# Performance work log

Measured on AMD Instinct MI355X. Metric: run time of the kernel, lower is better.

## Reference

```python
import jax, jax.numpy as jnp
import numpy as np

DIM_M = 512
NEG_INF = -1e30


def setup_inputs() -> dict:
    key = jax.random.key(0)
    k1, k2, k3, k4, k5, k6, k7 = jax.random.split(key, 7)
    B, Lc, Lq, d = 16, 1024, 512, DIM_M
    C = jax.random.normal(k1, (B, Lc, d), dtype=jnp.float32)
    Q = jax.random.normal(k2, (B, Lq, d), dtype=jnp.float32)
    cmask = jax.random.randint(k3, (B, Lc), 0, 2).astype(jnp.float32)
    qmask = jax.random.randint(k4, (B, Lq), 0, 2).astype(jnp.float32)
    lim = np.sqrt(1.0 / d)
    w = jax.random.uniform(k5, (3 * d,), minval=-lim, maxval=lim, dtype=jnp.float32)
    # out_linear: Linear(4d -> d), torch default init
    bound = np.sqrt(1.0 / (4 * d))
    out_w = jax.random.uniform(k6, (d, 4 * d), minval=-bound, maxval=bound, dtype=jnp.float32)
    out_b = jax.random.uniform(k7, (d,), minval=-bound, maxval=bound, dtype=jnp.float32)
    return {"C": C, "Q": Q, "cmask": cmask, "qmask": qmask, "w": w, "out_w": out_w, "out_b": out_b}


def _mask_logits(t, m):
    return t * m + (1.0 - m) * NEG_INF


def reference(C, Q, cmask, qmask, w, out_w, out_b):
    d = C.shape[-1]
    w1, w2, w3 = w[:d], w[d:2 * d], w[2 * d:]
    # Decomposed trilinear similarity (same math as cat([Ct,Qt,Ct*Qt]) @ w):
    # S[b,i,j] = C[b,i]@w1 + Q[b,j]@w2 + (C[b,i]*w3) @ Q[b,j]
    S = (C @ w1)[:, :, None] + (Q @ w2)[:, None, :] \
        + jnp.einsum('bid,bjd->bij', C * w3, Q)  # [B, Lc, Lq]
    qm = qmask[:, None, :]  # [B, 1, Lq]
    cm = cmask[:, :, None]  # [B, Lc, 1]
    S1 = jax.nn.softmax(_mask_logits(S, qm), axis=2)  # over Lq
    S2 = jax.nn.softmax(_mask_logits(S, cm), axis=1)  # over Lc
    A = jnp.einsum('bij,bjd->bid', S1, Q)  # [B, Lc, d]
    # bmm(bmm(S1, S2^T), C) == S1 @ (S2^T @ C) by associativity (cheaper)
    S2TC = jnp.einsum('bij,bid->bjd', S2, C)  # [B, Lq, d]
    Bm = jnp.einsum('bij,bjd->bid', S1, S2TC)  # [B, Lc, d]
    out = jnp.concatenate([C, A, C * A, C * Bm], axis=2)  # [B, Lc, 4d]
    # dropout inactive (inference); out_linear
    return out @ out_w.T + out_b
```

## Files before the change

kernel.cpp:

```cpp
#include <hip/hip_runtime.h>
#include <hip/hip_bf16.h>


#define NB 16
#define LC 1024
#define LQ 512
#define DM 512
#define D4 2048
#define NEGINF (-1e30f)
#define LDA64 72
#define LDA32 40

typedef __bf16 v8bf __attribute__((ext_vector_type(8)));
typedef __bf16 v4bf __attribute__((ext_vector_type(4)));
typedef float  v4f  __attribute__((ext_vector_type(4)));

#define MFMA16 __builtin_amdgcn_mfma_f32_16x16x32_bf16

#define TILE_SETUP8 \
  const int t = threadIdx.x, lane = t & 63, wave = t >> 6; \
  const int wm = wave >> 2, wn = wave & 3, quad = lane >> 4, col = lane & 15; \
  const int sr = t >> 2;

#define ZERO_ACC8 \
  v4f acc[4][2]; \
  _Pragma("unroll") for (int x = 0; x < 4; ++x) \
  _Pragma("unroll") for (int y = 0; y < 2; ++y) \
  _Pragma("unroll") for (int r = 0; r < 4; ++r) acc[x][y][r] = 0.f;

#define FRAG_MMA8S(AL, BL, LDA, KO) do { \
  v8bf af_[4], bf_[2]; \
  _Pragma("unroll") for (int x = 0; x < 4; ++x) \
    af_[x] = *(const v8bf*)&AL[(wm * 64 + x * 16 + col) * LDA + KO + quad * 8]; \
  _Pragma("unroll") for (int y = 0; y < 2; ++y) \
    bf_[y] = *(const v8bf*)&BL[(wn * 32 + y * 16 + col) * LDA + KO + quad * 8]; \
  _Pragma("unroll") for (int x = 0; x < 4; ++x) \
  _Pragma("unroll") for (int y = 0; y < 2; ++y) \
    acc[x][y] = MFMA16(af_[x], bf_[y], acc[x][y], 0, 0, 0); \
} while (0)

__device__ __forceinline__ void xcd_remap(int& bx, int& by, int& bz) {
  const int gx = gridDim.x, gy = gridDim.y, gz = gridDim.z;
  int flat = bx + gx * (by + gy * bz);
  int per = (gx * gy * gz) >> 3;
  int nw = (flat & 7) * per + (flat >> 3);
  bx = nw % gx;
  int r = nw / gx;
  by = r % gy;
  bz = r / gy;
}

__device__ __forceinline__ v8bf cvt8f(float4 a, float4 b) {
  v8bf h;
  h[0] = (__bf16)a.x; h[1] = (__bf16)a.y; h[2] = (__bf16)a.z; h[3] = (__bf16)a.w;
  h[4] = (__bf16)b.x; h[5] = (__bf16)b.y; h[6] = (__bf16)b.z; h[7] = (__bf16)b.w;
  return h;
}

__global__ void k_rowdots(const float* __restrict__ C, const float* __restrict__ Q,
                          const float* __restrict__ w,
                          float* __restrict__ cw1, float* __restrict__ qw2) {
  const int wid = threadIdx.x >> 6, lane = threadIdx.x & 63;
  const int row = blockIdx.x * 4 + wid;
  const bool isC = row < NB * LC;
  const float* src = isC ? (C + (size_t)row * DM) : (Q + (size_t)(row - NB * LC) * DM);
  const float* wv  = isC ? w : (w + DM);
  float v = 0.f;
#pragma unroll
  for (int tt = 0; tt < 8; ++tt) {
    int k = lane + 64 * tt;
    v += src[k] * wv[k];
  }
#pragma unroll
  for (int off = 32; off; off >>= 1) v += __shfl_down(v, off, 64);
  if (lane == 0) {
    if (isC) cw1[row] = v;
    else     qw2[row - NB * LC] = v;
  }
}

__global__ void k_transpose(const float* __restrict__ in, __bf16* __restrict__ outT,
                            int R, int Cd) {
  __shared__ __bf16 tile[64][66];
  const int b = blockIdx.z;
  const int r0 = blockIdx.y * 64, c0 = blockIdx.x * 64;
  const int tr = threadIdx.x >> 6, tc = threadIdx.x & 63;
  const float* inb = in + (size_t)b * R * Cd;
  __bf16* outb = outT + (size_t)b * Cd * R;
  for (int r = tr; r < 64; r += 4)
    tile[r][tc] = (__bf16)inb[(size_t)(r0 + r) * Cd + c0 + tc];
  __syncthreads();
  for (int c = tr; c < 64; c += 4)
    outb[(size_t)(c0 + c) * R + r0 + tc] = tile[tc][c];
}

__global__ void k_owcvt(const float* __restrict__ OW, __bf16* __restrict__ OWb) {
  size_t i = ((size_t)blockIdx.x * 256 + threadIdx.x) * 4;
  float4 f = *(const float4*)(OW + i);
  v4bf h; h[0] = (__bf16)f.x; h[1] = (__bf16)f.y; h[2] = (__bf16)f.z; h[3] = (__bf16)f.w;
  *(v4bf*)(OWb + i) = h;
}

__global__ __launch_bounds__(512) void k_mfma_S(
    const float* __restrict__ C, const float* __restrict__ Q, const float* __restrict__ w,
    const float* __restrict__ cw1, const float* __restrict__ qw2, float* __restrict__ S) {
  __shared__ __bf16 Al[128 * LDA64], Bl[128 * LDA64];
  int bx = blockIdx.x, by = blockIdx.y, bz = blockIdx.z;
  xcd_remap(bx, by, bz);
  const int b = bz, i0 = by * 128, j0 = bx * 128;
  TILE_SETUP8
  const int skc = (t & 3) * 16;
  const float* Cb = C + (size_t)b * LC * DM;
  const float* Qb = Q + (size_t)b * LQ * DM;
  const float* w3 = w + 2 * DM;
  float4 pc[4], pq[4];
  auto load = [&](int k0) {
    const float* ca = Cb + (size_t)(i0 + sr) * DM + k0 + skc;
    const float* qa = Qb + (size_t)(j0 + sr) * DM + k0 + skc;
#pragma unroll
    for (int u = 0; u < 4; ++u) {
      pc[u] = *(const float4*)(ca + 4 * u);
      pq[u] = *(const float4*)(qa + 4 * u);
    }
  };
  load(0);
  ZERO_ACC8
  for (int k0 = 0; k0 < DM; k0 += 64) {
    const float* wa = w3 + k0 + skc;
#pragma unroll
    for (int u = 0; u < 2; ++u) {
      float4 c0 = pc[2 * u], c1 = pc[2 * u + 1];
      float4 w0 = *(const float4*)(wa + 8 * u), w1 = *(const float4*)(wa + 8 * u + 4);
      v8bf ah;
      ah[0] = (__bf16)(c0.x * w0.x); ah[1] = (__bf16)(c0.y * w0.y);
      ah[2] = (__bf16)(c0.z * w0.z); ah[3] = (__bf16)(c0.w * w0.w);
      ah[4] = (__bf16)(c1.x * w1.x); ah[5] = (__bf16)(c1.y * w1.y);
      ah[6] = (__bf16)(c1.z * w1.z); ah[7] = (__bf16)(c1.w * w1.w);
      *(v8bf*)&Al[sr * LDA64 + skc + 8 * u] = ah;
      *(v8bf*)&Bl[sr * LDA64 + skc + 8 * u] = cvt8f(pq[2 * u], pq[2 * u + 1]);
    }
    __syncthreads();
    int kn = k0 + 64; if (kn >= DM) kn = 0;
    load(kn);
    FRAG_MMA8S(Al, Bl, LDA64, 0);
    FRAG_MMA8S(Al, Bl, LDA64, 32);
    __syncthreads();
  }
  float* Sb = S + (size_t)b * LC * LQ;
#pragma unroll
  for (int x = 0; x < 4; ++x) {
    const int mB = i0 + wm * 64 + x * 16 + quad * 4;
    float cv[4];
#pragma unroll
    for (int r = 0; r < 4; ++r) cv[r] = cw1[b * LC + mB + r];
#pragma unroll
    for (int y = 0; y < 2; ++y) {
      const int j = j0 + wn * 32 + y * 16 + col;
      const float qv = qw2[b * LQ + j];
#pragma unroll
      for (int r = 0; r < 4; ++r)
        Sb[(size_t)(mB + r) * LQ + j] = acc[x][y][r] + cv[r] + qv;
    }
  }
}

__global__ __launch_bounds__(1024) void k_softstat(
    const float* __restrict__ S, const float* __restrict__ qmask,
    const float* __restrict__ cmask, __bf16* __restrict__ S1,
    float2* __restrict__ pstat) {
  __shared__ float2 cst[16][LQ];
  const int b = blockIdx.y, ic = blockIdx.x;
  const int tid = threadIdx.x, wv = tid >> 6, lane = tid & 63;
  const float* qm  = qmask + b * LQ;
  const float* cm  = cmask + b * LC + ic * 64;
  const float* Sb  = S  + ((size_t)b * LC + ic * 64) * LQ;
  __bf16*      S1b = S1 + ((size_t)b * LC + ic * 64) * LQ;
  float colm[8], cols[8];
#pragma unroll
  for (int tt = 0; tt < 8; ++tt) { colm[tt] = -3e38f; cols[tt] = 0.f; }
  for (int it = 0; it < 4; ++it) {
    const int r = wv * 4 + it;
    const float cmv = cm[r];
    const float* Srow = Sb + (size_t)r * LQ;
    float sv[8], l1[8];
    float m = -3e38f;
#pragma unroll
    for (int tt = 0; tt < 8; ++tt) {
      int j = lane + 64 * tt;
      sv[tt] = Srow[j];
      float qv = qm[j];
      l1[tt] = qv * sv[tt] + (1.f - qv) * NEGINF;
      m = fmaxf(m, l1[tt]);
    }
#pragma unroll
    for (int off = 32; off; off >>= 1) m = fmaxf(m, __shfl_xor(m, off, 64));
    float e[8], s = 0.f;
#pragma unroll
    for (int tt = 0; tt < 8; ++tt) { e[tt] = __expf(l1[tt] - m); s += e[tt]; }
#pragma unroll
    for (int off = 32; off; off >>= 1) s += __shfl_xor(s, off, 64);
    const float inv = 1.f / s;
#pragma unroll
    for (int tt = 0; tt < 8; ++tt)
      S1b[(size_t)r * LQ + lane + 64 * tt] = (__bf16)(e[tt] * inv);
#pragma unroll
    for (int tt = 0; tt < 8; ++tt) {
      float l2 = cmv * sv[tt] + (1.f - cmv) * NEGINF;
      if (l2 > colm[tt]) { cols[tt] *= __expf(colm[tt] - l2); colm[tt] = l2; }
      cols[tt] += __expf(l2 - colm[tt]);
    }
  }
#pragma unroll
  for (int tt = 0; tt < 8; ++tt) cst[wv][lane + 64 * tt] = make_float2(colm[tt], cols[tt]);
  __syncthreads();
  if (tid < LQ) {
    float M = -3e38f, Sd = 0.f;
#pragma unroll
    for (int k = 0; k < 16; ++k) {
      float2 p = cst[k][tid];
      float nM = fmaxf(M, p.x);
      Sd = Sd * __expf(M - nM) + p.y * __expf(p.x - nM);
      M = nM;
    }
    pstat[((size_t)(b * 16 + ic) * LQ) + tid] = make_float2(M, Sd);
  }
}

__global__ void k_colwrite(const float* __restrict__ S, const float* __restrict__ cmask,
                           const float2* __restrict__ pstat, __bf16* __restrict__ S2T) {
  __shared__ float Mf[64], If[64];
  __shared__ __bf16 tile[64][66];
  const int b = blockIdx.z, ic = blockIdx.y, j0 = blockIdx.x * 64;
  const int c = threadIdx.x & 63, ip = threadIdx.x >> 6;
  if (threadIdx.x < 64) {
    float M = -3e38f, Sd = 0.f;
#pragma unroll
    for (int k = 0; k < 16; ++k) {
      float2 p = pstat[((size_t)(b * 16 + k) * LQ) + j0 + threadIdx.x];
      float nM = fmaxf(M, p.x);
      Sd = Sd * __expf(M - nM) + p.y * __expf(p.x - nM);
      M = nM;
    }
    Mf[threadIdx.x] = M; If[threadIdx.x] = 1.f / Sd;
  }
  __syncthreads();
  const float M = Mf[c], inv = If[c];
  const float* Sb = S + ((size_t)b * LC + ic * 64) * LQ;
  const float* cm = cmask + b * LC + ic * 64;
  for (int r = ip; r < 64; r += 4) {
    float mk = cm[r];
    float logit = mk * Sb[(size_t)r * LQ + j0 + c] + (1.f - mk) * NEGINF;
    tile[r][c] = (__bf16)(__expf(logit - M) * inv);
  }
  __syncthreads();
  __bf16* S2Tb = S2T + ((size_t)b * LQ + j0) * LC + ic * 64;
  for (int jr = ip; jr < 64; jr += 4)
    S2Tb[(size_t)jr * LC + c] = tile[c][jr];
}

__global__ __launch_bounds__(512) void k_mfma_A(
    const __bf16* __restrict__ S1, const __bf16* __restrict__ QT, __bf16* __restrict__ Aw) {
  __shared__ __bf16 Al[128 * LDA64], Bl[128 * LDA64];
  int bx = blockIdx.x, by = blockIdx.y, bz = blockIdx.z;
  xcd_remap(bx, by, bz);
  const int b = bz, i0 = by * 128, n0 = bx * 128;
  TILE_SETUP8
  const int skc = (t & 3) * 16;
  const __bf16* Ar = S1 + (size_t)b * LC * LQ + (size_t)(i0 + sr) * LQ + skc;
  const __bf16* Br = QT + (size_t)b * DM * LQ + (size_t)(n0 + sr) * LQ + skc;
  v8bf pa0, pa1, pb0, pb1;
  auto load = [&](int k0) {
    pa0 = *(const v8bf*)(Ar + k0); pa1 = *(const v8bf*)(Ar + k0 + 8);
    pb0 = *(const v8bf*)(Br + k0); pb1 = *(const v8bf*)(Br + k0 + 8);
  };
  load(0);
  ZERO_ACC8
  for (int k0 = 0; k0 < LQ; k0 += 64) {
    *(v8bf*)&Al[sr * LDA64 + skc] = pa0; *(v8bf*)&Al[sr * LDA64 + skc + 8] = pa1;
    *(v8bf*)&Bl[sr * LDA64 + skc] = pb0; *(v8bf*)&Bl[sr * LDA64 + skc + 8] = pb1;
    __syncthreads();
    int kn = k0 + 64; if (kn >= LQ) kn = 0;
    load(kn);
    FRAG_MMA8S(Al, Bl, LDA64, 0);
    FRAG_MMA8S(Al, Bl, LDA64, 32);
    __syncthreads();
  }
  __bf16* Ab = Aw + (size_t)b * LC * DM;
#pragma unroll
  for (int x = 0; x < 4; ++x) {
    const int mB = i0 + wm * 64 + x * 16 + quad * 4;
#pragma unroll
    for (int y = 0; y < 2; ++y) {
      const int n = n0 + wn * 32 + y * 16 + col;
#pragma unroll
      for (int r = 0; r < 4; ++r)
        Ab[(size_t)(mB + r) * DM + n] = (__bf16)acc[x][y][r];
    }
  }
}

__global__ __launch_bounds__(512) void k_mfma_T(
    const __bf16* __restrict__ S2T, const __bf16* __restrict__ CT, __bf16* __restrict__ S2TCT) {
  __shared__ __bf16 Al[128 * LDA64], Bl[128 * LDA64];
  int bx = blockIdx.x, by = blockIdx.y, bz = blockIdx.z;
  xcd_remap(bx, by, bz);
  const int b = bz, j0 = by * 128, n0 = bx * 128;
  TILE_SETUP8
  const int skc = (t & 3) * 16;
  const __bf16* Ar = S2T + (size_t)b * LQ * LC + (size_t)(j0 + sr) * LC + skc;
  const __bf16* Br = CT  + (size_t)b * DM * LC + (size_t)(n0 + sr) * LC + skc;
  v8bf pa0, pa1, pb0, pb1;
  auto load = [&](int k0) {
    pa0 = *(const v8bf*)(Ar + k0); pa1 = *(const v8bf*)(Ar + k0 + 8);
    pb0 = *(const v8bf*)(Br + k0); pb1 = *(const v8bf*)(Br + k0 + 8);
  };
  load(0);
  ZERO_ACC8
  for (int k0 = 0; k0 < LC; k0 += 64) {
    *(v8bf*)&Al[sr * LDA64 + skc] = pa0; *(v8bf*)&Al[sr * LDA64 + skc + 8] = pa1;
    *(v8bf*)&Bl[sr * LDA64 + skc] = pb0; *(v8bf*)&Bl[sr * LDA64 + skc + 8] = pb1;
    __syncthreads();
    int kn = k0 + 64; if (kn >= LC) kn = 0;
    load(kn);
    FRAG_MMA8S(Al, Bl, LDA64, 0);
    FRAG_MMA8S(Al, Bl, LDA64, 32);
    __syncthreads();
  }
#pragma unroll
  for (int x = 0; x < 4; ++x) {
    const int jB = j0 + wm * 64 + x * 16 + quad * 4;
#pragma unroll
    for (int y = 0; y < 2; ++y) {
      const int n = n0 + wn * 32 + y * 16 + col;
      v4bf h;
#pragma unroll
      for (int r = 0; r < 4; ++r) h[r] = (__bf16)acc[x][y][r];
      *(v4bf*)&S2TCT[((size_t)b * DM + n) * LQ + jB] = h;
    }
  }
}

__global__ __launch_bounds__(512) void k_mfma_Bm(
    const __bf16* __restrict__ S1, const __bf16* __restrict__ S2TCT, __bf16* __restrict__ Bmw) {
  __shared__ __bf16 Al[128 * LDA64], Bl[128 * LDA64];
  int bx = blockIdx.x, by = blockIdx.y, bz = blockIdx.z;
  xcd_remap(bx, by, bz);
  const int b = bz, i0 = by * 128, n0 = bx * 128;
  TILE_SETUP8
  const int skc = (t & 3) * 16;
  const __bf16* Ar = S1    + (size_t)b * LC * LQ + (size_t)(i0 + sr) * LQ + skc;
  const __bf16* Br = S2TCT + (size_t)b * DM * LQ + (size_t)(n0 + sr) * LQ + skc;
  v8bf pa0, pa1, pb0, pb1;
  auto load = [&](int k0) {
    pa0 = *(const v8bf*)(Ar + k0); pa1 = *(const v8bf*)(Ar + k0 + 8);
    pb0 = *(const v8bf*)(Br + k0); pb1 = *(const v8bf*)(Br + k0 + 8);
  };
  load(0);
  ZERO_ACC8
  for (int k0 = 0; k0 < LQ; k0 += 64) {
    *(v8bf*)&Al[sr * LDA64 + skc] = pa0; *(v8bf*)&Al[sr * LDA64 + skc + 8] = pa1;
    *(v8bf*)&Bl[sr * LDA64 + skc] = pb0; *(v8bf*)&Bl[sr * LDA64 + skc + 8] = pb1;
    __syncthreads();
    int kn = k0 + 64; if (kn >= LQ) kn = 0;
    load(kn);
    FRAG_MMA8S(Al, Bl, LDA64, 0);
    FRAG_MMA8S(Al, Bl, LDA64, 32);
    __syncthreads();
  }
  __bf16* Bb = Bmw + (size_t)b * LC * DM;
#pragma unroll
  for (int x = 0; x < 4; ++x) {
    const int mB = i0 + wm * 64 + x * 16 + quad * 4;
#pragma unroll
    for (int y = 0; y < 2; ++y) {
      const int n = n0 + wn * 32 + y * 16 + col;
#pragma unroll
      for (int r = 0; r < 4; ++r)
        Bb[(size_t)(mB + r) * DM + n] = (__bf16)acc[x][y][r];
    }
  }
}

__global__ __launch_bounds__(512) void k_mfma_out(
    const float* __restrict__ C, const __bf16* __restrict__ Aw, const __bf16* __restrict__ Bmw,
    const __bf16* __restrict__ OWb, const float* __restrict__ ob, float* __restrict__ out) {
  __shared__ __bf16 Asg[4][128 * LDA32], Bsg[4][128 * LDA32];
  int bx = blockIdx.x, by = blockIdx.y, bz = blockIdx.z;
  xcd_remap(bx, by, bz);
  const int b = bz, i0 = by * 128, n0 = bx * 128;
  TILE_SETUP8
  const int skc = (t & 3) * 8;
  const float*  Cr = C   + (size_t)b * LC * DM + (size_t)(i0 + sr) * DM + skc;
  const __bf16* Ar = Aw  + (size_t)b * LC * DM + (size_t)(i0 + sr) * DM + skc;
  const __bf16* Br = Bmw + (size_t)b * LC * DM + (size_t)(i0 + sr) * DM + skc;
  const __bf16* Wr = OWb + (size_t)(n0 + sr) * D4 + skc;
  float4 pc0, pc1; v8bf pA, pB, pw[4];
  auto load = [&](int kl) {
    pc0 = *(const float4*)(Cr + kl); pc1 = *(const float4*)(Cr + kl + 4);
    pA = *(const v8bf*)(Ar + kl);
    pB = *(const v8bf*)(Br + kl);
#pragma unroll
    for (int s = 0; s < 4; ++s) pw[s] = *(const v8bf*)(Wr + s * DM + kl);
  };
  load(0);
  ZERO_ACC8
  for (int kl = 0; kl < DM; kl += 32) {
    float cf[8] = {pc0.x, pc0.y, pc0.z, pc0.w, pc1.x, pc1.y, pc1.z, pc1.w};
    v8bf hC, hCA, hCB;
#pragma unroll
    for (int e = 0; e < 8; ++e) {
      hC[e]  = (__bf16)cf[e];
      hCA[e] = (__bf16)(cf[e] * (float)pA[e]);
      hCB[e] = (__bf16)(cf[e] * (float)pB[e]);
    }
    const int off = sr * LDA32 + skc;
    *(v8bf*)&Asg[0][off] = hC;
    *(v8bf*)&Asg[1][off] = pA;
    *(v8bf*)&Asg[2][off] = hCA;
    *(v8bf*)&Asg[3][off] = hCB;
#pragma unroll
    for (int s = 0; s < 4; ++s) *(v8bf*)&Bsg[s][off] = pw[s];
    __syncthreads();
    int kn = kl + 32; if (kn >= DM) kn = 0;
    load(kn);
#pragma unroll
    for (int s = 0; s < 4; ++s) FRAG_MMA8S(Asg[s], Bsg[s], LDA32, 0);
    __syncthreads();
  }
  float* outb = out + (size_t)b * LC * DM;
#pragma unroll
  for (int x = 0; x < 4; ++x) {
    const int mB = i0 + wm * 64 + x * 16 + quad * 4;
#pragma unroll
    for (int y = 0; y < 2; ++y) {
      const int n = n0 + wn * 32 + y * 16 + col;
      const float bv = ob[n];
#pragma unroll
      for (int r = 0; r < 4; ++r)
        outb[(size_t)(mB + r) * DM + n] = acc[x][y][r] + bv;
    }
  }
}

extern "C" void kernel_launch(void* const* d_in, const int* in_sizes, int n_in,
                              void* d_out, int out_size, void* d_ws, size_t ws_size,
                              hipStream_t stream) {
  const float* C     = (const float*)d_in[0];
  const float* Q     = (const float*)d_in[1];
  const float* cmask = (const float*)d_in[2];
  const float* qmask = (const float*)d_in[3];
  const float* w     = (const float*)d_in[4];
  const float* out_w = (const float*)d_in[5];
  const float* out_b = (const float*)d_in[6];
  float* out = (float*)d_out;

  char* base = (char*)d_ws;
  float*  cw1   = (float*)base;
  float*  qw2   = (float*)(base + 65536);
  char*   R     = base + 131072;
  float*  S     = (float*)R;
  __bf16* Aw    = (__bf16*)R;
  __bf16* CT    = (__bf16*)(R + (16u << 20));
  __bf16* Bmw   = (__bf16*)(R + (16u << 20));
  __bf16* S1    = (__bf16*)(base + 131072 + (32u << 20));
  __bf16* S2T   = (__bf16*)(base + 131072 + (48u << 20));
  __bf16* OWbf  = S2T;
  char*   Z     = base + 131072 + (64u << 20);
  float2* pstat = (float2*)Z;
  __bf16* QT    = (__bf16*)Z;
  __bf16* S2TCT = (__bf16*)Z;
  (void)in_sizes; (void)n_in; (void)out_size; (void)ws_size;

  k_rowdots<<<(NB * LC + NB * LQ) / 4, 256, 0, stream>>>(C, Q, w, cw1, qw2);
  k_mfma_S<<<dim3(LQ / 128, LC / 128, NB), 512, 0, stream>>>(C, Q, w, cw1, qw2, S);
  k_softstat<<<dim3(LC / 64, NB), 1024, 0, stream>>>(S, qmask, cmask, S1, pstat);
  k_colwrite<<<dim3(LQ / 64, LC / 64, NB), 256, 0, stream>>>(S, cmask, pstat, S2T);
  k_transpose<<<dim3(DM / 64, LQ / 64, NB), 256, 0, stream>>>(Q, QT, LQ, DM);
  k_transpose<<<dim3(DM / 64, LC / 64, NB), 256, 0, stream>>>(C, CT, LC, DM);
  k_mfma_A<<<dim3(DM / 128, LC / 128, NB), 512, 0, stream>>>(S1, QT, Aw);
  k_mfma_T<<<dim3(DM / 128, LQ / 128, NB), 512, 0, stream>>>(S2T, CT, S2TCT);
  k_owcvt<<<DM * D4 / 1024, 256, 0, stream>>>(out_w, OWbf);
  k_mfma_Bm<<<dim3(DM / 128, LC / 128, NB), 512, 0, stream>>>(S1, S2TCT, Bmw);
  k_mfma_out<<<dim3(DM / 128, LC / 128, NB), 512, 0, stream>>>(C, Aw, Bmw, OWbf, out_b, out);
}
```

Before: 283.0 us.

## Use direct global-to-LDS loads in shared bf16 GEMM macro with 4x4 wave tiles

```diff
diff --git a/kernel.cpp b/kernel.cpp
--- a/kernel.cpp
+++ b/kernel.cpp
@@ -8,7 +8,6 @@
 #define DM 512
 #define D4 2048
 #define NEGINF (-1e30f)
-#define LDA64 72
 #define LDA32 40
 
 typedef __bf16 v8bf __attribute__((ext_vector_type(8)));
@@ -16,6 +15,10 @@
 typedef float  v4f  __attribute__((ext_vector_type(4)));
 
 #define MFMA16 __builtin_amdgcn_mfma_f32_16x16x32_bf16
+
+#define GLOAD16(gp, lp) __builtin_amdgcn_global_load_lds( \
+    (const __attribute__((address_space(1))) void*)(gp), \
+    (__attribute__((address_space(3))) void*)(lp), 16, 0, 0)
 
 #define TILE_SETUP8 \
   const int t = threadIdx.x, lane = t & 63, wave = t >> 6; \
@@ -39,6 +42,39 @@
     acc[x][y] = MFMA16(af_[x], bf_[y], acc[x][y], 0, 0, 0); \
 } while (0)
 
+#define GEMM_PROLOG \
+  __shared__ __bf16 Al[128 * 64], Bl[128 * 64]; \
+  int bx = blockIdx.x, by = blockIdx.y, bz = blockIdx.z; \
+  xcd_remap(bx, by, bz); \
+  const int b = bz, i0 = by * 128, n0 = bx * 128; \
+  const int t = threadIdx.x, lane = t & 63, wave = t >> 6; \
+  const int wm = wave >> 1, wn = wave & 1, quad = lane >> 4, col = lane & 15; \
+  const int srow = wave * 32 + (lane >> 3), scol = (lane & 7) * 8; \
+  v4f acc[4][4]; \
+  _Pragma("unroll") for (int x = 0; x < 4; ++x) \
+  _Pragma("unroll") for (int y = 0; y < 4; ++y) \
+  _Pragma("unroll") for (int r = 0; r < 4; ++r) acc[x][y][r] = 0.f;
+
+#define GEMM_KLOOP(Arow, Brow, LDGA, LDGB, KEXT) \
+  for (int k0 = 0; k0 < (KEXT); k0 += 64) { \
+    _Pragma("unroll") for (int u = 0; u < 4; ++u) { \
+      GLOAD16(Arow + (size_t)(u * 8) * (LDGA) + k0, &Al[(wave * 32 + u * 8) * 64]); \
+      GLOAD16(Brow + (size_t)(u * 8) * (LDGB) + k0, &Bl[(wave * 32 + u * 8) * 64]); \
+    } \
+    __syncthreads(); \
+    _Pragma("unroll") for (int ko = 0; ko < 2; ++ko) { \
+      v8bf af_[4], bf_[4]; \
+      _Pragma("unroll") for (int x = 0; x < 4; ++x) \
+        af_[x] = *(const v8bf*)&Al[(wm * 64 + x * 16 + col) * 64 + ko * 32 + quad * 8]; \
+      _Pragma("unroll") for (int y = 0; y < 4; ++y) \
+        bf_[y] = *(const v8bf*)&Bl[(wn * 64 + y * 16 + col) * 64 + ko * 32 + quad * 8]; \
+      _Pragma("unroll") for (int x = 0; x < 4; ++x) \
+      _Pragma("unroll") for (int y = 0; y < 4; ++y) \
+        acc[x][y] = MFMA16(af_[x], bf_[y], acc[x][y], 0, 0, 0); \
+    } \
+    __syncthreads(); \
+  }
+
 __device__ __forceinline__ void xcd_remap(int& bx, int& by, int& bz) {
   const int gx = gridDim.x, gy = gridDim.y, gz = gridDim.z;
   int flat = bx + gx * (by + gy * bz);
@@ -59,23 +95,38 @@
 
 __global__ void k_rowdots(const float* __restrict__ C, const float* __restrict__ Q,
                           const float* __restrict__ w,
-                          float* __restrict__ cw1, float* __restrict__ qw2) {
+                          float* __restrict__ cw1, float* __restrict__ qw2,
+                          __bf16* __restrict__ Cbf, __bf16* __restrict__ Qw3) {
   const int wid = threadIdx.x >> 6, lane = threadIdx.x & 63;
   const int row = blockIdx.x * 4 + wid;
   const bool isC = row < NB * LC;
-  const float* src = isC ? (C + (size_t)row * DM) : (Q + (size_t)(row - NB * LC) * DM);
+  const int lr = isC ? row : row - NB * LC;
+  const float* src = (isC ? C : Q) + (size_t)lr * DM;
   const float* wv  = isC ? w : (w + DM);
+  const float* w3  = w + 2 * DM;
+  __bf16* dst = (isC ? Cbf : Qw3) + (size_t)lr * DM;
   float v = 0.f;
 #pragma unroll
-  for (int tt = 0; tt < 8; ++tt) {
-    int k = lane + 64 * tt;
-    v += src[k] * wv[k];
+  for (int s = 0; s < 2; ++s) {
+    const int k = lane * 4 + s * 256;
+    float4 f = *(const float4*)(src + k);
+    float4 g = *(const float4*)(wv + k);
+    v += f.x * g.x + f.y * g.y + f.z * g.z + f.w * g.w;
+    v4bf h;
+    if (isC) {
+      h[0] = (__bf16)f.x; h[1] = (__bf16)f.y; h[2] = (__bf16)f.z; h[3] = (__bf16)f.w;
+    } else {
+      float4 s3 = *(const float4*)(w3 + k);
+      h[0] = (__bf16)(f.x * s3.x); h[1] = (__bf16)(f.y * s3.y);
+      h[2] = (__bf16)(f.z * s3.z); h[3] = (__bf16)(f.w * s3.w);
+    }
+    *(v4bf*)(dst + k) = h;
   }
 #pragma unroll
   for (int off = 32; off; off >>= 1) v += __shfl_down(v, off, 64);
   if (lane == 0) {
     if (isC) cw1[row] = v;
-    else     qw2[row - NB * LC] = v;
+    else     qw2[lr] = v;
   }
 }
 
@@ -101,51 +152,14 @@
   *(v4bf*)(OWb + i) = h;
 }
 
-__global__ __launch_bounds__(512) void k_mfma_S(
-    const float* __restrict__ C, const float* __restrict__ Q, const float* __restrict__ w,
-    const float* __restrict__ cw1, const float* __restrict__ qw2, float* __restrict__ S) {
-  __shared__ __bf16 Al[128 * LDA64], Bl[128 * LDA64];
-  int bx = blockIdx.x, by = blockIdx.y, bz = blockIdx.z;
-  xcd_remap(bx, by, bz);
-  const int b = bz, i0 = by * 128, j0 = bx * 128;
-  TILE_SETUP8
-  const int skc = (t & 3) * 16;
-  const float* Cb = C + (size_t)b * LC * DM;
-  const float* Qb = Q + (size_t)b * LQ * DM;
-  const float* w3 = w + 2 * DM;
-  float4 pc[4], pq[4];
-  auto load = [&](int k0) {
-    const float* ca = Cb + (size_t)(i0 + sr) * DM + k0 + skc;
-    const float* qa = Qb + (size_t)(j0 + sr) * DM + k0 + skc;
-#pragma unroll
-    for (int u = 0; u < 4; ++u) {
-      pc[u] = *(const float4*)(ca + 4 * u);
-      pq[u] = *(const float4*)(qa + 4 * u);
-    }
-  };
-  load(0);
-  ZERO_ACC8
-  for (int k0 = 0; k0 < DM; k0 += 64) {
-    const float* wa = w3 + k0 + skc;
-#pragma unroll
-    for (int u = 0; u < 2; ++u) {
-      float4 c0 = pc[2 * u], c1 = pc[2 * u + 1];
-      float4 w0 = *(const float4*)(wa + 8 * u), w1 = *(const float4*)(wa + 8 * u + 4);
-      v8bf ah;
-      ah[0] = (__bf16)(c0.x * w0.x); ah[1] = (__bf16)(c0.y * w0.y);
-      ah[2] = (__bf16)(c0.z * w0.z); ah[3] = (__bf16)(c0.w * w0.w);
-      ah[4] = (__bf16)(c1.x * w1.x); ah[5] = (__bf16)(c1.y * w1.y);
-      ah[6] = (__bf16)(c1.z * w1.z); ah[7] = (__bf16)(c1.w * w1.w);
-      *(v8bf*)&Al[sr * LDA64 + skc + 8 * u] = ah;
-      *(v8bf*)&Bl[sr * LDA64 + skc + 8 * u] = cvt8f(pq[2 * u], pq[2 * u + 1]);
-    }
-    __syncthreads();
-    int kn = k0 + 64; if (kn >= DM) kn = 0;
-    load(kn);
-    FRAG_MMA8S(Al, Bl, LDA64, 0);
-    FRAG_MMA8S(Al, Bl, LDA64, 32);
-    __syncthreads();
-  }
+__global__ __launch_bounds__(256) void k_mfma_S(
+    const __bf16* __restrict__ Cbf, const __bf16* __restrict__ Qw3,
+    const float* __restrict__ cw1, const float* __restrict__ qw2,
+    float* __restrict__ S) {
+  GEMM_PROLOG
+  const __bf16* Arow = Cbf + (size_t)b * LC * DM + (size_t)(i0 + srow) * DM + scol;
+  const __bf16* Brow = Qw3 + (size_t)b * LQ * DM + (size_t)(n0 + srow) * DM + scol;
+  GEMM_KLOOP(Arow, Brow, DM, DM, DM)
   float* Sb = S + (size_t)b * LC * LQ;
 #pragma unroll
   for (int x = 0; x < 4; ++x) {
@@ -154,8 +168,8 @@
 #pragma unroll
     for (int r = 0; r < 4; ++r) cv[r] = cw1[b * LC + mB + r];
 #pragma unroll
-    for (int y = 0; y < 2; ++y) {
-      const int j = j0 + wn * 32 + y * 16 + col;
+    for (int y = 0; y < 4; ++y) {
+      const int j = n0 + wn * 64 + y * 16 + col;
       const float qv = qw2[b * LQ + j];
 #pragma unroll
       for (int r = 0; r < 4; ++r)
@@ -258,40 +272,19 @@
     S2Tb[(size_t)jr * LC + c] = tile[c][jr];
 }
 
-__global__ __launch_bounds__(512) void k_mfma_A(
+__global__ __launch_bounds__(256) void k_mfma_A(
     const __bf16* __restrict__ S1, const __bf16* __restrict__ QT, __bf16* __restrict__ Aw) {
-  __shared__ __bf16 Al[128 * LDA64], Bl[128 * LDA64];
-  int bx = blockIdx.x, by = blockIdx.y, bz = blockIdx.z;
-  xcd_remap(bx, by, bz);
-  const int b = bz, i0 = by * 128, n0 = bx * 128;
-  TILE_SETUP8
-  const int skc = (t & 3) * 16;
-  const __bf16* Ar = S1 + (size_t)b * LC * LQ + (size_t)(i0 + sr) * LQ + skc;
-  const __bf16* Br = QT + (size_t)b * DM * LQ + (size_t)(n0 + sr) * LQ + skc;
-  v8bf pa0, pa1, pb0, pb1;
-  auto load = [&](int k0) {
-    pa0 = *(const v8bf*)(Ar + k0); pa1 = *(const v8bf*)(Ar + k0 + 8);
-    pb0 = *(const v8bf*)(Br + k0); pb1 = *(const v8bf*)(Br + k0 + 8);
-  };
-  load(0);
-  ZERO_ACC8
-  for (int k0 = 0; k0 < LQ; k0 += 64) {
-    *(v8bf*)&Al[sr * LDA64 + skc] = pa0; *(v8bf*)&Al[sr * LDA64 + skc + 8] = pa1;
-    *(v8bf*)&Bl[sr * LDA64 + skc] = pb0; *(v8bf*)&Bl[sr * LDA64 + skc + 8] = pb1;
-    __syncthreads();
-    int kn = k0 + 64; if (kn >= LQ) kn = 0;
-    load(kn);
-    FRAG_MMA8S(Al, Bl, LDA64, 0);
-    FRAG_MMA8S(Al, Bl, LDA64, 32);
-    __syncthreads();
-  }
+  GEMM_PROLOG
+  const __bf16* Arow = S1 + (size_t)b * LC * LQ + (size_t)(i0 + srow) * LQ + scol;
+  const __bf16* Brow = QT + (size_t)b * DM * LQ + (size_t)(n0 + srow) * LQ + scol;
+  GEMM_KLOOP(Arow, Brow, LQ, LQ, LQ)
   __bf16* Ab = Aw + (size_t)b * LC * DM;
 #pragma unroll
   for (int x = 0; x < 4; ++x) {
     const int mB = i0 + wm * 64 + x * 16 + quad * 4;
 #pragma unroll
-    for (int y = 0; y < 2; ++y) {
-      const int n = n0 + wn * 32 + y * 16 + col;
+    for (int y = 0; y < 4; ++y) {
+      const int n = n0 + wn * 64 + y * 16 + col;
 #pragma unroll
       for (int r = 0; r < 4; ++r)
         Ab[(size_t)(mB + r) * DM + n] = (__bf16)acc[x][y][r];
@@ -299,39 +292,19 @@
   }
 }
 
-__global__ __launch_bounds__(512) void k_mfma_T(
+__global__ __launch_bounds__(256) void k_mfma_T(
     const __bf16* __restrict__ S2T, const __bf16* __restrict__ CT, __bf16* __restrict__ S2TCT) {
-  __shared__ __bf16 Al[128 * LDA64], Bl[128 * LDA64];
-  int bx = blockIdx.x, by = blockIdx.y, bz = blockIdx.z;
-  xcd_remap(bx, by, bz);
-  const int b = bz, j0 = by * 128, n0 = bx * 128;
-  TILE_SETUP8
-  const int skc = (t & 3) * 16;
-  const __bf16* Ar = S2T + (size_t)b * LQ * LC + (size_t)(j0 + sr) * LC + skc;
-  const __bf16* Br = CT  + (size_t)b * DM * LC + (size_t)(n0 + sr) * LC + skc;
-  v8bf pa0, pa1, pb0, pb1;
-  auto load = [&](int k0) {
-    pa0 = *(const v8bf*)(Ar + k0); pa1 = *(const v8bf*)(Ar + k0 + 8);
-    pb0 = *(const v8bf*)(Br + k0); pb1 = *(const v8bf*)(Br + k0 + 8);
-  };
-  load(0);
-  ZERO_ACC8
-  for (int k0 = 0; k0 < LC; k0 += 64) {
-    *(v8bf*)&Al[sr * LDA64 + skc] = pa0; *(v8bf*)&Al[sr * LDA64 + skc + 8] = pa1;
-    *(v8bf*)&Bl[sr * LDA64 + skc] = pb0; *(v8bf*)&Bl[sr * LDA64 + skc + 8] = pb1;
-    __syncthreads();
-    int kn = k0 + 64; if (kn >= LC) kn = 0;
-    load(kn);
-    FRAG_MMA8S(Al, Bl, LDA64, 0);
-    FRAG_MMA8S(Al, Bl, LDA64, 32);
-    __syncthreads();
-  }
+  GEMM_PROLOG
+  const int j0 = i0;
+  const __bf16* Arow = S2T + (size_t)b * LQ * LC + (size_t)(j0 + srow) * LC + scol;
+  const __bf16* Brow = CT  + (size_t)b * DM * LC + (size_t)(n0 + srow) * LC + scol;
+  GEMM_KLOOP(Arow, Brow, LC, LC, LC)
 #pragma unroll
   for (int x = 0; x < 4; ++x) {
     const int jB = j0 + wm * 64 + x * 16 + quad * 4;
 #pragma unroll
-    for (int y = 0; y < 2; ++y) {
-      const int n = n0 + wn * 32 + y * 16 + col;
+    for (int y = 0; y < 4; ++y) {
+      const int n = n0 + wn * 64 + y * 16 + col;
       v4bf h;
 #pragma unroll
       for (int r = 0; r < 4; ++r) h[r] = (__bf16)acc[x][y][r];
@@ -340,40 +313,19 @@
   }
 }
 
-__global__ __launch_bounds__(512) void k_mfma_Bm(
+__global__ __launch_bounds__(256) void k_mfma_Bm(
     const __bf16* __restrict__ S1, const __bf16* __restrict__ S2TCT, __bf16* __restrict__ Bmw) {
-  __shared__ __bf16 Al[128 * LDA64], Bl[128 * LDA64];
-  int bx = blockIdx.x, by = blockIdx.y, bz = blockIdx.z;
-  xcd_remap(bx, by, bz);
-  const int b = bz, i0 = by * 128, n0 = bx * 128;
-  TILE_SETUP8
-  const int skc = (t & 3) * 16;
-  const __bf16* Ar = S1    + (size_t)b * LC * LQ + (size_t)(i0 + sr) * LQ + skc;
-  const __bf16* Br = S2TCT + (size_t)b * DM * LQ + (size_t)(n0 + sr) * LQ + skc;
-  v8bf pa0, pa1, pb0, pb1;
-  auto load = [&](int k0) {
-    pa0 = *(const v8bf*)(Ar + k0); pa1 = *(const v8bf*)(Ar + k0 + 8);
-    pb0 = *(const v8bf*)(Br + k0); pb1 = *(const v8bf*)(Br + k0 + 8);
-  };
-  load(0);
-  ZERO_ACC8
-  for (int k0 = 0; k0 < LQ; k0 += 64) {
-    *(v8bf*)&Al[sr * LDA64 + skc] = pa0; *(v8bf*)&Al[sr * LDA64 + skc + 8] = pa1;
-    *(v8bf*)&Bl[sr * LDA64 + skc] = pb0; *(v8bf*)&Bl[sr * LDA64 + skc + 8] = pb1;
-    __syncthreads();
-    int kn = k0 + 64; if (kn >= LQ) kn = 0;
-    load(kn);
-    FRAG_MMA8S(Al, Bl, LDA64, 0);
-    FRAG_MMA8S(Al, Bl, LDA64, 32);
-    __syncthreads();
-  }
+  GEMM_PROLOG
+  const __bf16* Arow = S1    + (size_t)b * LC * LQ + (size_t)(i0 + srow) * LQ + scol;
+  const __bf16* Brow = S2TCT + (size_t)b * DM * LQ + (size_t)(n0 + srow) * LQ + scol;
+  GEMM_KLOOP(Arow, Brow, LQ, LQ, LQ)
   __bf16* Bb = Bmw + (size_t)b * LC * DM;
 #pragma unroll
   for (int x = 0; x < 4; ++x) {
     const int mB = i0 + wm * 64 + x * 16 + quad * 4;
 #pragma unroll
-    for (int y = 0; y < 2; ++y) {
-      const int n = n0 + wn * 32 + y * 16 + col;
+    for (int y = 0; y < 4; ++y) {
+      const int n = n0 + wn * 64 + y * 16 + col;
 #pragma unroll
       for (int r = 0; r < 4; ++r)
         Bb[(size_t)(mB + r) * DM + n] = (__bf16)acc[x][y][r];
@@ -462,7 +414,9 @@
   __bf16* Aw    = (__bf16*)R;
   __bf16* CT    = (__bf16*)(R + (16u << 20));
   __bf16* Bmw   = (__bf16*)(R + (16u << 20));
+  __bf16* Cbf   = (__bf16*)(base + 131072 + (32u << 20));
   __bf16* S1    = (__bf16*)(base + 131072 + (32u << 20));
+  __bf16* Qw3   = (__bf16*)(base + 131072 + (48u << 20));
   __bf16* S2T   = (__bf16*)(base + 131072 + (48u << 20));
   __bf16* OWbf  = S2T;
   char*   Z     = base + 131072 + (64u << 20);
@@ -471,15 +425,15 @@
   __bf16* S2TCT = (__bf16*)Z;
   (void)in_sizes; (void)n_in; (void)out_size; (void)ws_size;
 
-  k_rowdots<<<(NB * LC + NB * LQ) / 4, 256, 0, stream>>>(C, Q, w, cw1, qw2);
-  k_mfma_S<<<dim3(LQ / 128, LC / 128, NB), 512, 0, stream>>>(C, Q, w, cw1, qw2, S);
+  k_rowdots<<<(NB * LC + NB * LQ) / 4, 256, 0, stream>>>(C, Q, w, cw1, qw2, Cbf, Qw3);
+  k_mfma_S<<<dim3(LQ / 128, LC / 128, NB), 256, 0, stream>>>(Cbf, Qw3, cw1, qw2, S);
   k_softstat<<<dim3(LC / 64, NB), 1024, 0, stream>>>(S, qmask, cmask, S1, pstat);
   k_colwrite<<<dim3(LQ / 64, LC / 64, NB), 256, 0, stream>>>(S, cmask, pstat, S2T);
   k_transpose<<<dim3(DM / 64, LQ / 64, NB), 256, 0, stream>>>(Q, QT, LQ, DM);
   k_transpose<<<dim3(DM / 64, LC / 64, NB), 256, 0, stream>>>(C, CT, LC, DM);
-  k_mfma_A<<<dim3(DM / 128, LC / 128, NB), 512, 0, stream>>>(S1, QT, Aw);
-  k_mfma_T<<<dim3(DM / 128, LQ / 128, NB), 512, 0, stream>>>(S2T, CT, S2TCT);
+  k_mfma_A<<<dim3(DM / 128, LC / 128, NB), 256, 0, stream>>>(S1, QT, Aw);
+  k_mfma_T<<<dim3(DM / 128, LQ / 128, NB), 256, 0, stream>>>(S2T, CT, S2TCT);
   k_owcvt<<<DM * D4 / 1024, 256, 0, stream>>>(out_w, OWbf);
-  k_mfma_Bm<<<dim3(DM / 128, LC / 128, NB), 512, 0, stream>>>(S1, S2TCT, Bmw);
+  k_mfma_Bm<<<dim3(DM / 128, LC / 128, NB), 256, 0, stream>>>(S1, S2TCT, Bmw);
   k_mfma_out<<<dim3(DM / 128, LC / 128, NB), 512, 0, stream>>>(C, Aw, Bmw, OWbf, out_b, out);
 }
```

New measurement: 277.0 us. 1.02x faster.
